# Kernel tuning notes

Hardware: AMD Instinct MI355X
Metric: run time of the kernel (lower is better)

## Reference

```python
import jax, jax.numpy as jnp
import numpy as np

# Dims: N=batch graphs, V=grid nodes (128x128), D=feature dim, E=edges, L=gnn layers
N, V, D, E, L = 16, 16384, 128, 65536, 2
EPS = 1e-5  # BatchNorm1d default eps


def setup_inputs() -> dict:
    key = jax.random.key(0)
    ks = jax.random.split(key, 8)
    H = jax.random.normal(ks[0], (N, V, D), dtype=jnp.float32)
    edge_src = jax.random.randint(ks[1], (E,), 0, V, dtype=jnp.int32)
    edge_dst = jax.random.randint(ks[2], (E,), 0, V, dtype=jnp.int32)
    A_vals = jax.random.uniform(ks[3], (E,), dtype=jnp.float32)
    scale = 1.0 / np.sqrt(D).astype(np.float32)
    # Stacked per-layer params. Linear stores weight as [out, in]; y = x @ W.T
    W_self = jax.random.normal(ks[4], (L, D, D), dtype=jnp.float32) * scale
    W_nei = jax.random.normal(ks[5], (L, D, D), dtype=jnp.float32) * scale
    gamma = jnp.ones((L, D), dtype=jnp.float32)
    beta = jnp.zeros((L, D), dtype=jnp.float32)
    return {"H": H, "edge_src": edge_src, "edge_dst": edge_dst, "A_vals": A_vals,
            "W_self": W_self, "W_nei": W_nei, "gamma": gamma, "beta": beta}


def reference(H, edge_src, edge_dst, A_vals, W_self, W_nei, gamma, beta):
    X = H  # [N, V, D]
    for l in range(L):
        # SpMM: X_nei[n] = A_norm @ X[n], batched over N via vmap.
        msg = X[:, edge_src, :] * A_vals[None, :, None]  # [N, E, D]
        X_nei = jax.vmap(
            lambda m: jax.ops.segment_sum(m, edge_dst, num_segments=V)
        )(msg)  # [N, V, D]
        # y = x @ W.T for torch Linear(weight=[out,in])
        Y = (jnp.einsum('nvd,ed->nve', X, W_self[l])
             + jnp.einsum('nvd,ed->nve', X_nei, W_nei[l]))  # [N, V, D]
        # BatchNorm1d in training mode over the flattened (N*V) batch dim
        mean = jnp.mean(Y, axis=(0, 1))            # [D]
        var = jnp.var(Y, axis=(0, 1))              # biased variance, [D]
        Y = (Y - mean) * jax.lax.rsqrt(var + EPS) * gamma[l] + beta[l]
        X = jax.nn.relu(Y)
    return X
```

## Files before the change

kernel.cpp:

```cpp
#include <hip/hip_runtime.h>

#define N_ 16
#define V_ 16384
#define D_ 128
#define E_ 65536
#define L_ 2
#define M_ (N_*V_)

typedef __attribute__((ext_vector_type(8))) short short8;
typedef __attribute__((ext_vector_type(4))) float floatx4;

__device__ inline unsigned short f2bf(float x){
  unsigned u = __builtin_bit_cast(unsigned, x);
  unsigned r = u + 0x7fffu + ((u >> 16) & 1u);
  return (unsigned short)(r >> 16);
}
__device__ inline float bf2f(unsigned short h){
  unsigned u = ((unsigned)h) << 16;
  return __builtin_bit_cast(float, u);
}
__device__ inline unsigned pack2(float a, float b){
  return (unsigned)f2bf(a) | ((unsigned)f2bf(b) << 16);
}

__global__ __launch_bounds__(256) void conv_in_k(const float* __restrict__ H,
                                                 unsigned short* __restrict__ Xb){
  int i = blockIdx.x * 256 + threadIdx.x;
  const float4* h4 = (const float4*)H;
  float4 a = h4[2*i], b = h4[2*i+1];
  uint4 o;
  o.x = pack2(a.x, a.y);
  o.y = pack2(a.z, a.w);
  o.z = pack2(b.x, b.y);
  o.w = pack2(b.z, b.w);
  ((uint4*)Xb)[i] = o;
}

__global__ __launch_bounds__(256) void conv_w_k(const float* __restrict__ Wself,
                                                const float* __restrict__ Wnei,
                                                unsigned short* __restrict__ Wb){
  int f = blockIdx.x * 256 + threadIdx.x;
  int lane = f & 63;
  int ct   = (f >> 6) & 7;
  int ks   = (f >> 9) & 3;
  int mat  = (f >> 11) & 1;
  int l    = (f >> 12) & 1;
  int e = ct * 16 + (lane & 15);
  int d = ks * 32 + (lane >> 4) * 8;
  const float* src = (mat ? Wnei : Wself) + ((size_t)l * D_ * D_ + e * D_ + d);
  uint4 o;
  o.x = pack2(src[0], src[1]);
  o.y = pack2(src[2], src[3]);
  o.z = pack2(src[4], src[5]);
  o.w = pack2(src[6], src[7]);
  ((uint4*)Wb)[f] = o;
}

__global__ __launch_bounds__(256) void hist_k(const int* __restrict__ dst, int* __restrict__ cnt){
  int e = blockIdx.x * 256 + threadIdx.x;
  atomicAdd(&cnt[dst[e]], 1);
}

__global__ __launch_bounds__(256) void scan_k(const int* __restrict__ cnt, int* __restrict__ row_ptr){
  __shared__ int part[256];
  int t = threadIdx.x;
  int base = t * 64;
  int s = 0;
  for (int i = 0; i < 64; ++i) s += cnt[base + i];
  part[t] = s;
  __syncthreads();
  for (int d = 1; d < 256; d <<= 1){
    int v = (t >= d) ? part[t - d] : 0;
    __syncthreads();
    part[t] += v;
    __syncthreads();
  }
  int off = part[t] - s;
  for (int i = 0; i < 64; ++i){
    row_ptr[base + i] = off;
    off += cnt[base + i];
  }
  if (t == 255) row_ptr[V_] = off;
}

__global__ __launch_bounds__(256) void scatter_k(const int* __restrict__ src,
                                                 const int* __restrict__ dst,
                                                 const float* __restrict__ vals,
                                                 const int* __restrict__ row_ptr,
                                                 int* __restrict__ fill,
                                                 int* __restrict__ csr_col,
                                                 float* __restrict__ csr_val){
  int e = blockIdx.x * 256 + threadIdx.x;
  int d = dst[e];
  int pos = row_ptr[d] + atomicAdd(&fill[d], 1);
  csr_col[pos] = src[e];
  csr_val[pos] = vals[e];
}

template<int NORM>
__global__ __launch_bounds__(256) void spmm_k(const unsigned* __restrict__ X,
                                              const int* __restrict__ row_ptr,
                                              const int* __restrict__ csr_col,
                                              const float* __restrict__ csr_val,
                                              const float* __restrict__ scsh,
                                              unsigned* __restrict__ Xnei){
  int v = blockIdx.x;
  int tid = threadIdx.x;
  int wave = tid >> 6, lane = tid & 63;
  int l31 = lane & 31, nh = lane >> 5;
  float4 sc = {0.f,0.f,0.f,0.f}, sh = {0.f,0.f,0.f,0.f};
  if (NORM){
    sc = ((const float4*)scsh)[l31];
    sh = ((const float4*)(scsh + 128))[l31];
  }
  int r0 = row_ptr[v], r1 = row_ptr[v + 1];
  float acc[2][4] = {{0.f,0.f,0.f,0.f},{0.f,0.f,0.f,0.f}};
  for (int i = r0; i < r1; ++i){
    int c = csr_col[i];
    float a = csr_val[i];
#pragma unroll
    for (int p = 0; p < 2; ++p){
      int n = p * 8 + wave * 2 + nh;
      uint2 w = *((const uint2*)(X + ((size_t)n * V_ + c) * 64) + l31);
      float x0 = bf2f((unsigned short)(w.x & 0xffff));
      float x1 = bf2f((unsigned short)(w.x >> 16));
      float x2 = bf2f((unsigned short)(w.y & 0xffff));
      float x3 = bf2f((unsigned short)(w.y >> 16));
      if (NORM){
        x0 = fmaxf(0.f, x0 * sc.x + sh.x);
        x1 = fmaxf(0.f, x1 * sc.y + sh.y);
        x2 = fmaxf(0.f, x2 * sc.z + sh.z);
        x3 = fmaxf(0.f, x3 * sc.w + sh.w);
      }
      acc[p][0] += a * x0; acc[p][1] += a * x1;
      acc[p][2] += a * x2; acc[p][3] += a * x3;
    }
  }
#pragma unroll
  for (int p = 0; p < 2; ++p){
    int n = p * 8 + wave * 2 + nh;
    uint2 o;
    o.x = pack2(acc[p][0], acc[p][1]);
    o.y = pack2(acc[p][2], acc[p][3]);
    *((uint2*)(Xnei + ((size_t)n * V_ + v) * 64) + l31) = o;
  }
}

template<int NORM>
__global__ __launch_bounds__(256, 2) void gemm_k(const unsigned short* __restrict__ Xs,
                                                 const unsigned short* __restrict__ Xn,
                                                 const uint4* __restrict__ Wfrag,
                                                 const float* __restrict__ scsh,
                                                 unsigned short* __restrict__ Yb,
                                                 float* __restrict__ stats){
  __shared__ uint4 lds_w[4096];
  __shared__ float lds_s[256];
  int tid = threadIdx.x;
  for (int i = tid; i < 4096; i += 256) lds_w[i] = Wfrag[i];
  if (NORM) lds_s[tid] = scsh[tid];
  __syncthreads();

  int wave = tid >> 6, lane = tid & 63;
  int quad = lane >> 4, l15 = lane & 15;
  int row0 = blockIdx.x * 128 + wave * 32;

  floatx4 zero = {0.f, 0.f, 0.f, 0.f};
  floatx4 acc[2][8];
#pragma unroll
  for (int rt = 0; rt < 2; ++rt)
#pragma unroll
    for (int ct = 0; ct < 8; ++ct) acc[rt][ct] = zero;

  const short8* lw = (const short8*)lds_w;
#pragma unroll
  for (int ks = 0; ks < 4; ++ks){
    float scv[8], shv[8];
    if (NORM){
      int cb = ks * 32 + quad * 8;
#pragma unroll
      for (int j = 0; j < 8; ++j){
        scv[j] = lds_s[cb + j];
        shv[j] = lds_s[128 + cb + j];
      }
    }
    short8 a_s[2], a_n[2];
#pragma unroll
    for (int rt = 0; rt < 2; ++rt){
      size_t r = (size_t)(row0 + rt * 16 + l15);
      short8 raw = *(const short8*)(Xs + r * 128 + ks * 32 + quad * 8);
      if (NORM){
        short8 t;
#pragma unroll
        for (int j = 0; j < 8; ++j){
          float x = bf2f((unsigned short)raw[j]);
          x = fmaxf(0.f, x * scv[j] + shv[j]);
          t[j] = (short)f2bf(x);
        }
        a_s[rt] = t;
      } else {
        a_s[rt] = raw;
      }
      a_n[rt] = *(const short8*)(Xn + r * 128 + ks * 32 + quad * 8);
    }
#pragma unroll
    for (int ct = 0; ct < 8; ++ct){
      short8 bs = lw[((0 * 4 + ks) * 8 + ct) * 64 + lane];
      short8 bn = lw[((1 * 4 + ks) * 8 + ct) * 64 + lane];
#pragma unroll
      for (int rt = 0; rt < 2; ++rt){
        acc[rt][ct] = __builtin_amdgcn_mfma_f32_16x16x32_bf16(a_s[rt], bs, acc[rt][ct], 0, 0, 0);
        acc[rt][ct] = __builtin_amdgcn_mfma_f32_16x16x32_bf16(a_n[rt], bn, acc[rt][ct], 0, 0, 0);
      }
    }
  }

  float* sum_base = stats;
  float* sq_base  = stats + 64 * 128;
  int slot = blockIdx.x & 63;
#pragma unroll
  for (int rt = 0; rt < 2; ++rt){
    int rowq = row0 + rt * 16 + quad * 4;
#pragma unroll
    for (int ct = 0; ct < 8; ++ct){
      int col = ct * 16 + l15;
      float s = 0.f, q = 0.f;
#pragma unroll
      for (int rg = 0; rg < 4; ++rg){
        float yv = acc[rt][ct][rg];
        Yb[(size_t)(rowq + rg) * 128 + col] = f2bf(yv);
        s += yv; q += yv * yv;
      }
      s += __shfl_xor(s, 16); s += __shfl_xor(s, 32);
      q += __shfl_xor(q, 16); q += __shfl_xor(q, 32);
      if (lane < 16)      atomicAdd(&sum_base[slot * 128 + ct * 16 + lane], s);
      else if (lane < 32) atomicAdd(&sq_base [slot * 128 + ct * 16 + (lane & 15)], q);
    }
  }
}

__global__ __launch_bounds__(128) void finalize_k(const float* __restrict__ stats,
                                                  const float* __restrict__ gamma,
                                                  const float* __restrict__ beta,
                                                  float* __restrict__ scsh){
  int d = threadIdx.x;
  float s = 0.f, q = 0.f;
  for (int k = 0; k < 64; ++k){
    s += stats[k * 128 + d];
    q += stats[64 * 128 + k * 128 + d];
  }
  float inv = 1.0f / (float)M_;
  float mean = s * inv;
  float var  = q * inv - mean * mean;
  float rstd = rsqrtf(var + 1e-5f);
  float scale = gamma[d] * rstd;
  scsh[d]       = scale;
  scsh[128 + d] = beta[d] - mean * scale;
}

__global__ __launch_bounds__(256) void bn_out_k(const uint4* __restrict__ Y,
                                                const float* __restrict__ scsh,
                                                float4* __restrict__ out){
  int i = blockIdx.x * 256 + threadIdx.x;
  int c = (i * 8) & 127;
  uint4 y = Y[i];
  float4 sc0 = *(const float4*)(scsh + c);
  float4 sc1 = *(const float4*)(scsh + c + 4);
  float4 sh0 = *(const float4*)(scsh + 128 + c);
  float4 sh1 = *(const float4*)(scsh + 132 + c);
  float4 o0, o1;
  o0.x = fmaxf(0.f, bf2f((unsigned short)(y.x & 0xffff)) * sc0.x + sh0.x);
  o0.y = fmaxf(0.f, bf2f((unsigned short)(y.x >> 16))    * sc0.y + sh0.y);
  o0.z = fmaxf(0.f, bf2f((unsigned short)(y.y & 0xffff)) * sc0.z + sh0.z);
  o0.w = fmaxf(0.f, bf2f((unsigned short)(y.y >> 16))    * sc0.w + sh0.w);
  o1.x = fmaxf(0.f, bf2f((unsigned short)(y.z & 0xffff)) * sc1.x + sh1.x);
  o1.y = fmaxf(0.f, bf2f((unsigned short)(y.z >> 16))    * sc1.y + sh1.y);
  o1.z = fmaxf(0.f, bf2f((unsigned short)(y.w & 0xffff)) * sc1.z + sh1.z);
  o1.w = fmaxf(0.f, bf2f((unsigned short)(y.w >> 16))    * sc1.w + sh1.w);
  out[2 * i]     = o0;
  out[2 * i + 1] = o1;
}

static inline size_t align_up(size_t x, size_t a){ return (x + a - 1) & ~(a - 1); }

extern "C" void kernel_launch(void* const* d_in, const int* in_sizes, int n_in,
                              void* d_out, int out_size, void* d_ws, size_t ws_size,
                              hipStream_t stream){
  const float* H     = (const float*)d_in[0];
  const int*   esrc  = (const int*)  d_in[1];
  const int*   edst  = (const int*)  d_in[2];
  const float* avals = (const float*)d_in[3];
  const float* Wself = (const float*)d_in[4];
  const float* Wnei  = (const float*)d_in[5];
  const float* gamma = (const float*)d_in[6];
  const float* beta  = (const float*)d_in[7];

  char* ws = (char*)d_ws;
  size_t off = 0;
  unsigned short* Xb   = (unsigned short*)(ws + off); off += align_up((size_t)M_ * D_ * 2, 256);
  unsigned short* Xnei = (unsigned short*)(ws + off); off += align_up((size_t)M_ * D_ * 2, 256);
  unsigned short* Y0   = (unsigned short*)(ws + off); off += align_up((size_t)M_ * D_ * 2, 256);
  unsigned short* Wb   = (unsigned short*)(ws + off); off += align_up((size_t)L_ * 2 * D_ * D_ * 2, 256);
  int*   row_ptr = (int*)  (ws + off); off += align_up((size_t)(V_ + 1) * 4, 256);
  int*   csr_col = (int*)  (ws + off); off += align_up((size_t)E_ * 4, 256);
  float* csr_val = (float*)(ws + off); off += align_up((size_t)E_ * 4, 256);
  float* scsh0   = (float*)(ws + off); off += align_up((size_t)2 * 128 * 4, 256);
  float* scsh1   = (float*)(ws + off); off += align_up((size_t)2 * 128 * 4, 256);
  char* zbase = ws + off;
  int*   cnt    = (int*)  (ws + off); off += (size_t)V_ * 4;
  int*   fill   = (int*)  (ws + off); off += (size_t)V_ * 4;
  float* stats0 = (float*)(ws + off); off += (size_t)64 * 128 * 2 * 4;
  float* stats1 = (float*)(ws + off); off += (size_t)64 * 128 * 2 * 4;
  size_t zbytes = (size_t)(ws + off - zbase);
  unsigned short* Y1 = Xb;
  (void)ws_size; (void)in_sizes; (void)n_in; (void)out_size;

  conv_in_k<<<M_ * D_ / 8 / 256, 256, 0, stream>>>(H, Xb);
  conv_w_k<<<8192 / 256, 256, 0, stream>>>(Wself, Wnei, Wb);
  hipMemsetAsync(zbase, 0, zbytes, stream);
  hist_k<<<E_ / 256, 256, 0, stream>>>(edst, cnt);
  scan_k<<<1, 256, 0, stream>>>(cnt, row_ptr);
  scatter_k<<<E_ / 256, 256, 0, stream>>>(esrc, edst, avals, row_ptr, fill, csr_col, csr_val);

  spmm_k<0><<<V_, 256, 0, stream>>>((const unsigned*)Xb, row_ptr, csr_col, csr_val,
                                    nullptr, (unsigned*)Xnei);
  gemm_k<0><<<M_ / 128, 256, 0, stream>>>(Xb, Xnei, (const uint4*)Wb, nullptr, Y0, stats0);
  finalize_k<<<1, 128, 0, stream>>>(stats0, gamma, beta, scsh0);

  spmm_k<1><<<V_, 256, 0, stream>>>((const unsigned*)Y0, row_ptr, csr_col, csr_val,
                                    scsh0, (unsigned*)Xnei);
  gemm_k<1><<<M_ / 128, 256, 0, stream>>>(Y0, Xnei, (const uint4*)Wb + 4096, scsh0, Y1, stats1);
  finalize_k<<<1, 128, 0, stream>>>(stats1, gamma + 128, beta + 128, scsh1);
  bn_out_k<<<M_ * D_ / 8 / 256, 256, 0, stream>>>((const uint4*)Y1, scsh1, (float4*)d_out);
}
```

Before: 497.2 us.

## Switch internal activations to node-major layout for contiguous SpMM gathers

Internal bf16 activations are stored as [V][N][D] instead of [N][V][D]. Input conversion and output BN write are changed to transpose, and SpMM now gathers one contiguous 4KB row per neighbor with 16-byte loads. The aim is to replace scattered 256-byte reads across 16 graph slices with a single coalesced read per edge. The GEMM and BN stats are row-wise over M, so they stay valid under the permuted row order. The transposes in conv_in and bn_out may lose some write or read coalescing.

Result: no change. 505.8 us (+1.7%).

```diff
diff --git a/kernel.cpp b/kernel.cpp
--- a/kernel.cpp
+++ b/kernel.cpp
@@ -7,6 +7,7 @@
 #define L_ 2
 #define M_ (N_*V_)
 
+
 typedef __attribute__((ext_vector_type(8))) short short8;
 typedef __attribute__((ext_vector_type(4))) float floatx4;
 
@@ -25,15 +26,18 @@
 
 __global__ __launch_bounds__(256) void conv_in_k(const float* __restrict__ H,
                                                  unsigned short* __restrict__ Xb){
-  int i = blockIdx.x * 256 + threadIdx.x;
+  int v = blockIdx.x;
+  int t = threadIdx.x;
+  int n = t >> 4, dc = t & 15;
   const float4* h4 = (const float4*)H;
-  float4 a = h4[2*i], b = h4[2*i+1];
+  size_t base = ((size_t)n * V_ + v) * 32 + (size_t)dc * 2;
+  float4 a = h4[base], b = h4[base + 1];
   uint4 o;
   o.x = pack2(a.x, a.y);
   o.y = pack2(a.z, a.w);
   o.z = pack2(b.x, b.y);
   o.w = pack2(b.z, b.w);
-  ((uint4*)Xb)[i] = o;
+  ((uint4*)Xb)[(size_t)v * 256 + t] = o;
 }
 
 __global__ __launch_bounds__(256) void conv_w_k(const float* __restrict__ Wself,
@@ -98,52 +102,52 @@
 }
 
 template<int NORM>
-__global__ __launch_bounds__(256) void spmm_k(const unsigned* __restrict__ X,
+__global__ __launch_bounds__(256) void spmm_k(const uint4* __restrict__ X,
                                               const int* __restrict__ row_ptr,
                                               const int* __restrict__ csr_col,
                                               const float* __restrict__ csr_val,
                                               const float* __restrict__ scsh,
-                                              unsigned* __restrict__ Xnei){
+                                              uint4* __restrict__ Xnei){
   int v = blockIdx.x;
-  int tid = threadIdx.x;
-  int wave = tid >> 6, lane = tid & 63;
-  int l31 = lane & 31, nh = lane >> 5;
-  float4 sc = {0.f,0.f,0.f,0.f}, sh = {0.f,0.f,0.f,0.f};
+  int t = threadIdx.x;
+  float4 sc0 = {0,0,0,0}, sc1 = {0,0,0,0}, sh0 = {0,0,0,0}, sh1 = {0,0,0,0};
   if (NORM){
-    sc = ((const float4*)scsh)[l31];
-    sh = ((const float4*)(scsh + 128))[l31];
+    int d0 = (t & 15) * 8;
+    sc0 = *(const float4*)(scsh + d0);
+    sc1 = *(const float4*)(scsh + d0 + 4);
+    sh0 = *(const float4*)(scsh + 128 + d0);
+    sh1 = *(const float4*)(scsh + 128 + d0 + 4);
   }
   int r0 = row_ptr[v], r1 = row_ptr[v + 1];
-  float acc[2][4] = {{0.f,0.f,0.f,0.f},{0.f,0.f,0.f,0.f}};
+  float acc[8] = {0.f,0.f,0.f,0.f,0.f,0.f,0.f,0.f};
   for (int i = r0; i < r1; ++i){
     int c = csr_col[i];
     float a = csr_val[i];
-#pragma unroll
-    for (int p = 0; p < 2; ++p){
-      int n = p * 8 + wave * 2 + nh;
-      uint2 w = *((const uint2*)(X + ((size_t)n * V_ + c) * 64) + l31);
-      float x0 = bf2f((unsigned short)(w.x & 0xffff));
-      float x1 = bf2f((unsigned short)(w.x >> 16));
-      float x2 = bf2f((unsigned short)(w.y & 0xffff));
-      float x3 = bf2f((unsigned short)(w.y >> 16));
-      if (NORM){
-        x0 = fmaxf(0.f, x0 * sc.x + sh.x);
-        x1 = fmaxf(0.f, x1 * sc.y + sh.y);
-        x2 = fmaxf(0.f, x2 * sc.z + sh.z);
-        x3 = fmaxf(0.f, x3 * sc.w + sh.w);
-      }
-      acc[p][0] += a * x0; acc[p][1] += a * x1;
-      acc[p][2] += a * x2; acc[p][3] += a * x3;
-    }
-  }
-#pragma unroll
-  for (int p = 0; p < 2; ++p){
-    int n = p * 8 + wave * 2 + nh;
-    uint2 o;
-    o.x = pack2(acc[p][0], acc[p][1]);
-    o.y = pack2(acc[p][2], acc[p][3]);
-    *((uint2*)(Xnei + ((size_t)n * V_ + v) * 64) + l31) = o;
-  }
+    uint4 w = X[(size_t)c * 256 + t];
+    float x[8];
+    x[0] = bf2f((unsigned short)(w.x & 0xffff)); x[1] = bf2f((unsigned short)(w.x >> 16));
+    x[2] = bf2f((unsigned short)(w.y & 0xffff)); x[3] = bf2f((unsigned short)(w.y >> 16));
+    x[4] = bf2f((unsigned short)(w.z & 0xffff)); x[5] = bf2f((unsigned short)(w.z >> 16));
+    x[6] = bf2f((unsigned short)(w.w & 0xffff)); x[7] = bf2f((unsigned short)(w.w >> 16));
+    if (NORM){
+      x[0] = fmaxf(0.f, x[0] * sc0.x + sh0.x);
+      x[1] = fmaxf(0.f, x[1] * sc0.y + sh0.y);
+      x[2] = fmaxf(0.f, x[2] * sc0.z + sh0.z);
+      x[3] = fmaxf(0.f, x[3] * sc0.w + sh0.w);
+      x[4] = fmaxf(0.f, x[4] * sc1.x + sh1.x);
+      x[5] = fmaxf(0.f, x[5] * sc1.y + sh1.y);
+      x[6] = fmaxf(0.f, x[6] * sc1.z + sh1.z);
+      x[7] = fmaxf(0.f, x[7] * sc1.w + sh1.w);
+    }
+#pragma unroll
+    for (int j = 0; j < 8; ++j) acc[j] += a * x[j];
+  }
+  uint4 o;
+  o.x = pack2(acc[0], acc[1]);
+  o.y = pack2(acc[2], acc[3]);
+  o.z = pack2(acc[4], acc[5]);
+  o.w = pack2(acc[6], acc[7]);
+  Xnei[(size_t)v * 256 + t] = o;
 }
 
 template<int NORM>
@@ -260,13 +264,15 @@
 __global__ __launch_bounds__(256) void bn_out_k(const uint4* __restrict__ Y,
                                                 const float* __restrict__ scsh,
                                                 float4* __restrict__ out){
-  int i = blockIdx.x * 256 + threadIdx.x;
-  int c = (i * 8) & 127;
-  uint4 y = Y[i];
-  float4 sc0 = *(const float4*)(scsh + c);
-  float4 sc1 = *(const float4*)(scsh + c + 4);
-  float4 sh0 = *(const float4*)(scsh + 128 + c);
-  float4 sh1 = *(const float4*)(scsh + 132 + c);
+  int v = blockIdx.x;
+  int t = threadIdx.x;
+  int n = t >> 4, dc = t & 15;
+  uint4 y = Y[(size_t)v * 256 + t];
+  int d0 = dc * 8;
+  float4 sc0 = *(const float4*)(scsh + d0);
+  float4 sc1 = *(const float4*)(scsh + d0 + 4);
+  float4 sh0 = *(const float4*)(scsh + 128 + d0);
+  float4 sh1 = *(const float4*)(scsh + 128 + d0 + 4);
   float4 o0, o1;
   o0.x = fmaxf(0.f, bf2f((unsigned short)(y.x & 0xffff)) * sc0.x + sh0.x);
   o0.y = fmaxf(0.f, bf2f((unsigned short)(y.x >> 16))    * sc0.y + sh0.y);
@@ -276,8 +282,9 @@
   o1.y = fmaxf(0.f, bf2f((unsigned short)(y.z >> 16))    * sc1.y + sh1.y);
   o1.z = fmaxf(0.f, bf2f((unsigned short)(y.w & 0xffff)) * sc1.z + sh1.z);
   o1.w = fmaxf(0.f, bf2f((unsigned short)(y.w >> 16))    * sc1.w + sh1.w);
-  out[2 * i]     = o0;
-  out[2 * i + 1] = o1;
+  size_t ob = ((size_t)n * V_ + v) * 32 + (size_t)dc * 2;
+  out[ob]     = o0;
+  out[ob + 1] = o1;
 }
 
 static inline size_t align_up(size_t x, size_t a){ return (x + a - 1) & ~(a - 1); }
@@ -314,21 +321,21 @@
   unsigned short* Y1 = Xb;
   (void)ws_size; (void)in_sizes; (void)n_in; (void)out_size;
 
-  conv_in_k<<<M_ * D_ / 8 / 256, 256, 0, stream>>>(H, Xb);
+  conv_in_k<<<V_, 256, 0, stream>>>(H, Xb);
   conv_w_k<<<8192 / 256, 256, 0, stream>>>(Wself, Wnei, Wb);
   hipMemsetAsync(zbase, 0, zbytes, stream);
   hist_k<<<E_ / 256, 256, 0, stream>>>(edst, cnt);
   scan_k<<<1, 256, 0, stream>>>(cnt, row_ptr);
   scatter_k<<<E_ / 256, 256, 0, stream>>>(esrc, edst, avals, row_ptr, fill, csr_col, csr_val);
 
-  spmm_k<0><<<V_, 256, 0, stream>>>((const unsigned*)Xb, row_ptr, csr_col, csr_val,
-                                    nullptr, (unsigned*)Xnei);
+  spmm_k<0><<<V_, 256, 0, stream>>>((const uint4*)Xb, row_ptr, csr_col, csr_val,
+                                    nullptr, (uint4*)Xnei);
   gemm_k<0><<<M_ / 128, 256, 0, stream>>>(Xb, Xnei, (const uint4*)Wb, nullptr, Y0, stats0);
   finalize_k<<<1, 128, 0, stream>>>(stats0, gamma, beta, scsh0);
 
-  spmm_k<1><<<V_, 256, 0, stream>>>((const unsigned*)Y0, row_ptr, csr_col, csr_val,
-                                    scsh0, (unsigned*)Xnei);
+  spmm_k<1><<<V_, 256, 0, stream>>>((const uint4*)Y0, row_ptr, csr_col, csr_val,
+                                    scsh0, (uint4*)Xnei);
   gemm_k<1><<<M_ / 128, 256, 0, stream>>>(Y0, Xnei, (const uint4*)Wb + 4096, scsh0, Y1, stats1);
   finalize_k<<<1, 128, 0, stream>>>(stats1, gamma + 128, beta + 128, scsh1);
-  bn_out_k<<<M_ * D_ / 8 / 256, 256, 0, stream>>>((const uint4*)Y1, scsh1, (float4*)d_out);
-}
+  bn_out_k<<<V_, 256, 0, stream>>>((const uint4*)Y1, scsh1, (float4*)d_out);
+}
```
